# Kernel optimization log

Hardware: AMD Instinct MI355X
Metric: run time of the kernel (lower is better)

## Reference

```python
import jax, jax.numpy as jnp
import numpy as np

N_BATTERS = 20000
N_PITCHERS = 12000
SIT = 64          # situation_size
S = 256           # states per player row
N = N_BATTERS + N_PITCHERS
T = 8192          # number of at-bats (timesteps)
S2 = 2 * S


def setup_inputs() -> dict:
    key = jax.random.key(0)
    ks = jax.random.split(key, 10)
    x = jax.random.normal(ks[0], (T, SIT), dtype=jnp.float32)
    b = jax.random.randint(ks[1], (T,), 0, N)
    p = jax.random.randint(ks[2], (T,), 0, N)
    eye = jnp.eye(S2, dtype=jnp.float32)
    Wz = 0.05 * jax.random.normal(ks[3], (S2, SIT), dtype=jnp.float32)
    Wr = 0.05 * jax.random.normal(ks[4], (S2, SIT), dtype=jnp.float32)
    Wh = 0.05 * jax.random.normal(ks[5], (S2, SIT), dtype=jnp.float32)
    # original uses Identity(gain=0.8) init; small noise added for non-trivial grads
    Uz = 0.8 * eye + 0.02 * jax.random.normal(ks[6], (S2, S2), dtype=jnp.float32)
    Ur = 0.8 * eye + 0.02 * jax.random.normal(ks[7], (S2, S2), dtype=jnp.float32)
    Uh = 0.8 * eye + 0.02 * jax.random.normal(ks[8], (S2, S2), dtype=jnp.float32)
    bz = jnp.zeros((S2,), dtype=jnp.float32)
    br = jnp.ones((S2,), dtype=jnp.float32)
    bh = jnp.zeros((S2,), dtype=jnp.float32)
    table0 = 0.1 * jax.random.normal(ks[9], (N, S), dtype=jnp.float32)
    return dict(x=x, b=b, p=p, Wz=Wz, Wr=Wr, Wh=Wh, Uz=Uz, Ur=Ur, Uh=Uh,
                bz=bz, br=br, bh=bh, table0=table0)


def reference(x, b, p, Wz, Wr, Wh, Uz, Ur, Uh, bz, br, bh, table0):
    states = table0.shape[1]

    def step(table, inp):
        x_t, b_t, p_t = inp
        # gather batter and pitcher rows, concat to (2S,)
        h = jnp.concatenate([table[b_t], table[p_t]], axis=0)
        z = jax.nn.sigmoid(Wz @ x_t + Uz @ h + bz)
        r = jax.nn.sigmoid(Wr @ x_t + Ur @ h - br)   # note: minus br, as in source
        m = jnp.tanh(Wh @ x_t + Uh @ (r * h) + bh)
        hn = z * h + (1.0 - z) * m
        dh = (hn - h).reshape(2, states)
        # scatter-add deltas back (scatter_nd adds; duplicates accumulate)
        table = table.at[b_t].add(dh[0]).at[p_t].add(dh[1])
        return table, None

    final_table, _ = jax.lax.scan(step, table0, (x, b, p))
    return final_table
```

## Files before the change

### kernel.cpp

```cpp
#include <hip/hip_runtime.h>
#include <hip/hip_cooperative_groups.h>

namespace cg = cooperative_groups;

#define T_STEPS 8192
#define SIT     64
#define SS      256
#define S2      512
#define NPL     32000
#define NEV     (2*T_STEPS)
#define MAXLEV  255
#define RELAX   48
#define NKB     (S2/4)
#define WKB     (SIT/4)
#define BQMAX   16
#define CUTN    300
#define NSLICE  4
#define MAXB    4096
#define DIAG    0.8f

typedef __attribute__((ext_vector_type(8))) short short8;
typedef __attribute__((ext_vector_type(4))) float f32x4;

__device__ __forceinline__ float sigmoidf_(float x) {
    return 1.0f / (1.0f + expf(-x));
}
__device__ __forceinline__ float bflo_(unsigned u) { return __uint_as_float(u << 16); }
__device__ __forceinline__ float bfhi_(unsigned u) { return __uint_as_float(u & 0xFFFF0000u); }
__device__ __forceinline__ unsigned short f2bf_(float f) {
    unsigned u = __float_as_uint(f);
    u = u + 0x7FFFu + ((u >> 16) & 1u);
    return (unsigned short)(u >> 16);
}
__device__ __forceinline__ unsigned pk2_(float a, float b) {
    return (unsigned)f2bf_(a) | ((unsigned)f2bf_(b) << 16);
}
__device__ __forceinline__ float dot4_(float4 a, float4 b) {
    return a.x*b.x + a.y*b.y + a.z*b.z + a.w*b.w;
}
__device__ __forceinline__ float loadLLC_(const float* p) {
    return __hip_atomic_load(p, __ATOMIC_RELAXED, __HIP_MEMORY_SCOPE_AGENT);
}
__device__ __forceinline__ void storeLLC_(float* p, float v) {
    __hip_atomic_store(p, v, __ATOMIC_RELAXED, __HIP_MEMORY_SCOPE_AGENT);
}


__global__ void k_count(const int* __restrict__ b, const int* __restrict__ p, int* cnt) {
    int e = blockIdx.x * blockDim.x + threadIdx.x;
    if (e < NEV) {
        int v = (e & 1) ? p[e >> 1] : b[e >> 1];
        atomicAdd(&cnt[v], 1);
    }
}

__global__ __launch_bounds__(1024) void k_scan(const int* __restrict__ cnt, int* bas, int* cur) {
    __shared__ int partial[1024];
    int tid = threadIdx.x;
    int start = tid * 32;
    int end = start + 32; if (end > NPL) end = NPL;
    int s = 0;
    for (int i = start; i < end; ++i) s += cnt[i];
    partial[tid] = s;
    __syncthreads();
    for (int off = 1; off < 1024; off <<= 1) {
        int v = partial[tid];
        int add = (tid >= off) ? partial[tid - off] : 0;
        __syncthreads();
        partial[tid] = v + add;
        __syncthreads();
    }
    int acc = (tid == 0) ? 0 : partial[tid - 1];
    for (int i = start; i < end; ++i) {
        bas[i] = acc; cur[i] = acc; acc += cnt[i];
    }
}

__global__ void k_place(const int* __restrict__ b, const int* __restrict__ p, int* cur, int* list) {
    int e = blockIdx.x * blockDim.x + threadIdx.x;
    if (e < NEV) {
        int v = (e & 1) ? p[e >> 1] : b[e >> 1];
        int pos = atomicAdd(&cur[v], 1);
        list[pos] = e;
    }
}

__global__ void k_pred(const int* __restrict__ bas, const int* __restrict__ cnt, int* list, int* pred) {
    int v = blockIdx.x * blockDim.x + threadIdx.x;
    if (v >= NPL) return;
    int s0 = bas[v], c = cnt[v];
    for (int i2 = 1; i2 < c; ++i2) {
        int key = list[s0 + i2];
        int j = i2 - 1;
        while (j >= 0 && list[s0 + j] > key) { list[s0 + j + 1] = list[s0 + j]; --j; }
        list[s0 + j + 1] = key;
    }
    int prevS = -1, curS = -1;
    for (int i2 = 0; i2 < c; ++i2) {
        int e = list[s0 + i2];
        int s = e >> 1;
        if (s != curS) { prevS = curS; curS = s; }
        pred[e] = prevS;
    }
}

__global__ __launch_bounds__(1024) void k_levels(const int* __restrict__ pred,
                                                 int* order, int* levelStart, int* numLevels) {
    __shared__ short p0[T_STEPS], p1[T_STEPS];
    __shared__ unsigned char lev[T_STEPS];
    __shared__ int cnts[MAXLEV + 2];
    __shared__ int maxLev;
    __shared__ int changed;
    int tid = threadIdx.x;
    for (int t = tid; t < T_STEPS; t += 1024) {
        p0[t] = (short)pred[2 * t];
        p1[t] = (short)pred[2 * t + 1];
        lev[t] = 1;
    }
    for (int l = tid; l < MAXLEV + 2; l += 1024) cnts[l] = 0;
    if (tid == 0) maxLev = 0;
    __syncthreads();
    for (int r = 0; r < RELAX; ++r) {
        if (tid == 0) changed = 0;
        __syncthreads();
        for (int t = tid; t < T_STEPS; t += 1024) {
            int a = p0[t], b2 = p1[t];
            int la = (a >= 0) ? (int)lev[a] : 0;
            int lb = (b2 >= 0) ? (int)lev[b2] : 0;
            int nl = 1 + (la > lb ? la : lb);
            if (nl > MAXLEV) nl = MAXLEV;
            if (nl > (int)lev[t]) { lev[t] = (unsigned char)nl; changed = 1; }
        }
        __syncthreads();
        int ch = changed;
        __syncthreads();
        if (!ch) break;
    }
    for (int t = tid; t < T_STEPS; t += 1024) {
        atomicAdd(&cnts[lev[t]], 1);
        atomicMax(&maxLev, (int)lev[t]);
    }
    __syncthreads();
    if (tid == 0) {
        int acc = 0;
        levelStart[0] = 0;
        int cut = 0, stopped = 0;
        for (int l = 1; l <= maxLev; ++l) {
            int c = cnts[l];
            if (!stopped) { if (c > CUTN) cut = l; else stopped = 1; }
            cnts[l] = acc;
            acc += c;
            levelStart[l] = acc;
        }
        numLevels[0] = maxLev;
        numLevels[1] = cut;
    }
    __syncthreads();
    for (int t = tid; t < T_STEPS; t += 1024) {
        int pos = atomicAdd(&cnts[lev[t]], 1);
        order[pos] = t;
    }
}

__global__ void k_trans(const float* __restrict__ Uz, const float* __restrict__ Ur,
                        const float* __restrict__ Uh, const float* __restrict__ Wz,
                        const float* __restrict__ Wr, const float* __restrict__ Wh,
                        uint4* __restrict__ UzrP, uint2* __restrict__ UhP,
                        unsigned short* __restrict__ UBz, unsigned short* __restrict__ UBr,
                        unsigned short* __restrict__ UBh,
                        float* WzT, float* WrT, float* WhT) {
    int y = blockIdx.y;
    int idx = blockIdx.x * blockDim.x + threadIdx.x;
    if (y == 0) {
        if (idx < S2 * NKB) {
            int kb = idx >> 9, i2 = idx & (S2 - 1);
            int k = kb * 4;
            float z0 = Uz[i2 * S2 + k + 0] - ((i2 == k + 0) ? DIAG : 0.f);
            float z1 = Uz[i2 * S2 + k + 1] - ((i2 == k + 1) ? DIAG : 0.f);
            float z2 = Uz[i2 * S2 + k + 2] - ((i2 == k + 2) ? DIAG : 0.f);
            float z3 = Uz[i2 * S2 + k + 3] - ((i2 == k + 3) ? DIAG : 0.f);
            float r0 = Ur[i2 * S2 + k + 0] - ((i2 == k + 0) ? DIAG : 0.f);
            float r1 = Ur[i2 * S2 + k + 1] - ((i2 == k + 1) ? DIAG : 0.f);
            float r2 = Ur[i2 * S2 + k + 2] - ((i2 == k + 2) ? DIAG : 0.f);
            float r3 = Ur[i2 * S2 + k + 3] - ((i2 == k + 3) ? DIAG : 0.f);
            uint4 o;
            o.x = pk2_(z0, z1); o.y = pk2_(z2, z3);
            o.z = pk2_(r0, r1); o.w = pk2_(r2, r3);
            UzrP[idx] = o;
        }
    } else if (y == 1) {
        if (idx < S2 * NKB) {
            int kb = idx >> 9, i2 = idx & (S2 - 1);
            int k = kb * 4;
            float h0 = Uh[i2 * S2 + k + 0] - ((i2 == k + 0) ? DIAG : 0.f);
            float h1 = Uh[i2 * S2 + k + 1] - ((i2 == k + 1) ? DIAG : 0.f);
            float h2 = Uh[i2 * S2 + k + 2] - ((i2 == k + 2) ? DIAG : 0.f);
            float h3 = Uh[i2 * S2 + k + 3] - ((i2 == k + 3) ? DIAG : 0.f);
            uint2 o;
            o.x = pk2_(h0, h1); o.y = pk2_(h2, h3);
            UhP[idx] = o;
        }
    } else if (y <= 4) {
        const float* S = (y == 2) ? Wz : (y == 3) ? Wr : Wh;
        float*       D = (y == 2) ? WzT : (y == 3) ? WrT : WhT;
        if (idx < S2 * SIT) {
            int i2 = idx / SIT, k = idx % SIT;
            D[((k >> 2) * S2 + i2) * 4 + (k & 3)] = S[idx];
        }
    } else {
        const float* S = (y == 5) ? Uz : (y == 6) ? Ur : Uh;
        unsigned short* D = (y == 5) ? UBz : (y == 6) ? UBr : UBh;
        if (idx < S2 * S2) {
            int j = idx & 7;
            int lane = (idx >> 3) & 63;
            int ks = (idx >> 9) & 15;
            int nb = idx >> 13;
            int row = nb * 16 + (lane & 15);
            int col = ks * 32 + (lane >> 4) * 8 + j;
            float v = S[row * S2 + col] - ((row == col) ? DIAG : 0.f);
            D[idx] = f2bf_(v);
        }
    }
}

__global__ void k_copy(const float4* __restrict__ src, float4* dst, int n4) {
    int i = blockIdx.x * blockDim.x + threadIdx.x;
    if (i < n4) dst[i] = src[i];
}

__global__ __launch_bounds__(512) void k_xp(
    const float* __restrict__ x,
    const float* __restrict__ WzT, const float* __restrict__ WrT, const float* __restrict__ WhT,
    const float* __restrict__ bz, const float* __restrict__ br, const float* __restrict__ bh,
    float* __restrict__ XPz, float* __restrict__ XPr, float* __restrict__ XPh)
{
    __shared__ float xs[16][SIT];
    const int i = threadIdx.x;
    const int tile = blockIdx.x;
    const float4* Wz4 = (const float4*)WzT;
    const float4* Wr4 = (const float4*)WrT;
    const float4* Wh4 = (const float4*)WhT;
    const float bzi = bz[i], bri = br[i], bhi = bh[i];

    for (int idx = i; idx < 16 * SIT; idx += 512) {
        int j = idx >> 6, k = idx & (SIT - 1);
        xs[j][k] = x[(tile * 16 + j) * SIT + k];
    }
    __syncthreads();
    float za[16], ra[16], ha[16];
#pragma unroll
    for (int j = 0; j < 16; ++j) { za[j] = 0.f; ra[j] = 0.f; ha[j] = 0.f; }
    for (int kb = 0; kb < WKB; ++kb) {
        float4 wz = Wz4[kb * S2 + i];
        float4 wr = Wr4[kb * S2 + i];
        float4 wh = Wh4[kb * S2 + i];
#pragma unroll
        for (int j = 0; j < 16; ++j) {
            float4 x4 = *(const float4*)(&xs[j][kb * 4]);
            za[j] += dot4_(wz, x4);
            ra[j] += dot4_(wr, x4);
            ha[j] += dot4_(wh, x4);
        }
    }
#pragma unroll
    for (int j = 0; j < 16; ++j) {
        int t = tile * 16 + j;
        XPz[t * S2 + i] = za[j] + bzi;
        XPr[t * S2 + i] = ra[j] - bri;
        XPh[t * S2 + i] = ha[j] + bhi;
    }
}


__device__ __forceinline__ void tile_mfma(
    int sbase, int B, int i,
    const int* __restrict__ bArr, const int* __restrict__ pArr,
    const unsigned short* __restrict__ UBz, const unsigned short* __restrict__ UBr,
    const unsigned short* __restrict__ UBh,
    const float* __restrict__ XPz, const float* __restrict__ XPr, const float* __restrict__ XPh,
    float* __restrict__ out, const int* __restrict__ order,
    float* pool, int* tj, int* rbs, int* rps)
{
    unsigned short* Hbf  = (unsigned short*)(pool + 8192);
    unsigned short* RHbf = (unsigned short*)(pool + 12288);
    unsigned* H32 = (unsigned*)Hbf;
    const short8* BzF = (const short8*)UBz;
    const short8* BrF = (const short8*)UBr;
    const short8* BhF = (const short8*)UBh;
    const short8* AF  = (const short8*)Hbf;
    const short8* RF  = (const short8*)RHbf;
    const int lane = i & 63;
    const int w = i >> 6;

    __syncthreads();
    if (i < 16) {
        int t = (i < B) ? order[sbase + i] : -1;
        tj[i] = t;
        rbs[i] = (t >= 0) ? bArr[t] : 0;
        rps[i] = (t >= 0) ? pArr[t] : 0;
    }
    __syncthreads();

    for (int idx2 = i; idx2 < 16 * 256; idx2 += 512) {
        int j = idx2 >> 8, kp = (idx2 & 255) << 1;
        float v0 = 0.0f, v1 = 0.0f;
        if (tj[j] >= 0) {
            int row = (kp < SS) ? rbs[j] : rps[j];
            const float* rowp = out + row * SS + (kp & (SS - 1));
            v0 = rowp[0];
            v1 = rowp[1];
        }
        pool[j * S2 + kp] = v0;
        pool[j * S2 + kp + 1] = v1;
        int ks = kp >> 5, kk = kp & 31;
        H32[((((ks << 6) + j + ((kk >> 3) << 4)) << 3) + (kk & 7)) >> 1] = pk2_(v0, v1);
    }
    __syncthreads();

    f32x4 xpz[4], xpr[4];
#pragma unroll
    for (int nb2 = 0; nb2 < 4; ++nb2) {
        int c = (w * 4 + nb2) * 16 + (lane & 15);
#pragma unroll
        for (int q = 0; q < 4; ++q) {
            int m = ((lane >> 4) << 2) + q;
            int t = tj[m];
            xpz[nb2][q] = (t >= 0) ? XPz[t * S2 + c] : 0.f;
            xpr[nb2][q] = (t >= 0) ? XPr[t * S2 + c] : 0.f;
        }
    }

    f32x4 accz[4], accr[4];
#pragma unroll
    for (int nb2 = 0; nb2 < 4; ++nb2) {
        accz[nb2] = (f32x4){0.f, 0.f, 0.f, 0.f};
        accr[nb2] = (f32x4){0.f, 0.f, 0.f, 0.f};
    }
#pragma unroll 1
    for (int ks = 0; ks < 16; ++ks) {
        short8 a = AF[(ks << 6) + lane];
#pragma unroll
        for (int nb2 = 0; nb2 < 4; ++nb2) {
            int nb = w * 4 + nb2;
            short8 bz = BzF[((nb << 4) + ks) * 64 + lane];
            short8 br = BrF[((nb << 4) + ks) * 64 + lane];
            accz[nb2] = __builtin_amdgcn_mfma_f32_16x16x32_bf16(a, bz, accz[nb2], 0, 0, 0);
            accr[nb2] = __builtin_amdgcn_mfma_f32_16x16x32_bf16(a, br, accr[nb2], 0, 0, 0);
        }
    }
    f32x4 zv[4];
#pragma unroll
    for (int nb2 = 0; nb2 < 4; ++nb2) {
        int c = (w * 4 + nb2) * 16 + (lane & 15);
#pragma unroll
        for (int q = 0; q < 4; ++q) {
            int m = ((lane >> 4) << 2) + q;
            int t = tj[m];
            float h = pool[m * S2 + c];
            float zpre = accz[nb2][q] + xpz[nb2][q] + DIAG * h;
            float rpre = accr[nb2][q] + xpr[nb2][q] + DIAG * h;
            zv[nb2][q] = sigmoidf_(zpre);
            float rh = (t >= 0) ? sigmoidf_(rpre) * h : 0.f;
            int ks = c >> 5, kk = c & 31;
            RHbf[((ks << 6) + m + ((kk >> 3) << 4)) * 8 + (kk & 7)] = f2bf_(rh);
        }
    }
    __syncthreads();

    f32x4 xph[4];
#pragma unroll
    for (int nb2 = 0; nb2 < 4; ++nb2) {
        int c = (w * 4 + nb2) * 16 + (lane & 15);
#pragma unroll
        for (int q = 0; q < 4; ++q) {
            int m = ((lane >> 4) << 2) + q;
            int t = tj[m];
            xph[nb2][q] = (t >= 0) ? XPh[t * S2 + c] : 0.f;
        }
    }

    f32x4 accm[4];
#pragma unroll
    for (int nb2 = 0; nb2 < 4; ++nb2) accm[nb2] = (f32x4){0.f, 0.f, 0.f, 0.f};
#pragma unroll 1
    for (int ks = 0; ks < 16; ++ks) {
        short8 a = RF[(ks << 6) + lane];
#pragma unroll
        for (int nb2 = 0; nb2 < 4; ++nb2) {
            int nb = w * 4 + nb2;
            short8 bh = BhF[((nb << 4) + ks) * 64 + lane];
            accm[nb2] = __builtin_amdgcn_mfma_f32_16x16x32_bf16(a, bh, accm[nb2], 0, 0, 0);
        }
    }
#pragma unroll
    for (int nb2 = 0; nb2 < 4; ++nb2) {
        int c = (w * 4 + nb2) * 16 + (lane & 15);
#pragma unroll
        for (int q = 0; q < 4; ++q) {
            int m = ((lane >> 4) << 2) + q;
            int t = tj[m];
            if (t >= 0) {
                float h = pool[m * S2 + c];
                int ks = c >> 5, kk = c & 31;
                float rh = __uint_as_float(
                    ((unsigned)RHbf[((ks << 6) + m + ((kk >> 3) << 4)) * 8 + (kk & 7)]) << 16);
                float mm = tanhf(accm[nb2][q] + xph[nb2][q] + DIAG * rh);
                float z = zv[nb2][q];
                float hn = z * h + (1.f - z) * mm;
                int rb = rbs[m], rp = rps[m];
                int row = (c < SS) ? rb : rp;
                float* addr = out + row * SS + (c & (SS - 1));
                if (rb == rp) atomicAdd(addr, hn - h);
                else *addr = hn;
            }
        }
    }
}

template<int BQ>
__device__ __forceinline__ void process_level_valu(
    int s0, int s1, int i,
    const float* __restrict__ x,
    const int* __restrict__ bArr, const int* __restrict__ pArr,
    const float4* __restrict__ Wz4, const float4* __restrict__ Wr4, const float4* __restrict__ Wh4,
    const uint4* __restrict__ Uzr, const uint2* __restrict__ Uhp,
    float bzi, float bri, float bhi,
    float* __restrict__ out, const int* __restrict__ order,
    float* pool, int* tj, int* rbs, int* rps)
{
    float* Hsf = pool;
    float* RHf = pool + 8192;
    float* xsf = pool + 16384;
    const int nT = (s1 - s0 + BQ - 1) / BQ;
    for (int tile = blockIdx.x; tile < nT; tile += gridDim.x) {
        const int sbase = s0 + tile * BQ;
        const int B = (sbase + BQ <= s1) ? BQ : (s1 - sbase);
        __syncthreads();
        if (i < BQ) {
            int t = (i < B) ? order[sbase + i] : -1;
            tj[i] = t;
            rbs[i] = (t >= 0) ? bArr[t] : 0;
            rps[i] = (t >= 0) ? pArr[t] : 0;
        }
        __syncthreads();
        for (int idx = i; idx < BQ * S2; idx += 512) {
            int j = idx >> 9, k = idx & (S2 - 1);
            float v = 0.0f;
            if (tj[j] >= 0) {
                int row = (k < SS) ? rbs[j] : rps[j];
                v = out[row * SS + (k & (SS - 1))];
            }
            Hsf[j * S2 + k] = v;
        }
        for (int idx = i; idx < BQ * SIT; idx += 512) {
            int j = idx >> 6, k = idx & (SIT - 1);
            int t = tj[j];
            xsf[j * SIT + k] = (t >= 0) ? x[t * SIT + k] : 0.0f;
        }
        float zacc[BQ], racc[BQ];
#pragma unroll
        for (int j = 0; j < BQ; ++j) { zacc[j] = 0.0f; racc[j] = 0.0f; }
        __syncthreads();
        for (int kb = 0; kb < WKB; ++kb) {
            float4 a4 = Wz4[kb * S2 + i];
            float4 b4 = Wr4[kb * S2 + i];
#pragma unroll
            for (int j = 0; j < BQ; ++j) {
                float4 x4 = *(const float4*)(&xsf[j * SIT + kb * 4]);
                zacc[j] += dot4_(a4, x4);
                racc[j] += dot4_(b4, x4);
            }
        }
        for (int kb = 0; kb < NKB; ++kb) {
            uint4 u = Uzr[kb * S2 + i];
#pragma unroll
            for (int j = 0; j < BQ; ++j) {
                float4 h4 = *(const float4*)(&Hsf[j * S2 + kb * 4]);
                zacc[j] += bflo_(u.x) * h4.x + bfhi_(u.x) * h4.y + bflo_(u.y) * h4.z + bfhi_(u.y) * h4.w;
                racc[j] += bflo_(u.z) * h4.x + bfhi_(u.z) * h4.y + bflo_(u.w) * h4.z + bfhi_(u.w) * h4.w;
            }
        }
        float zv[BQ];
#pragma unroll
        for (int j = 0; j < BQ; ++j) {
            float hOwn = Hsf[j * S2 + i];
            zv[j] = sigmoidf_(zacc[j] + DIAG * hOwn + bzi);
            RHf[j * S2 + i] = sigmoidf_(racc[j] + DIAG * hOwn - bri) * hOwn;
        }
        __syncthreads();
        float macc[BQ];
#pragma unroll
        for (int j = 0; j < BQ; ++j) macc[j] = 0.0f;
        for (int kb = 0; kb < WKB; ++kb) {
            float4 a4 = Wh4[kb * S2 + i];
#pragma unroll
            for (int j = 0; j < BQ; ++j) {
                float4 x4 = *(const float4*)(&xsf[j * SIT + kb * 4]);
                macc[j] += dot4_(a4, x4);
            }
        }
        for (int kb = 0; kb < NKB; ++kb) {
            uint2 u = Uhp[kb * S2 + i];
#pragma unroll
            for (int j = 0; j < BQ; ++j) {
                float4 h4 = *(const float4*)(&RHf[j * S2 + kb * 4]);
                macc[j] += bflo_(u.x) * h4.x + bfhi_(u.x) * h4.y + bflo_(u.y) * h4.z + bfhi_(u.y) * h4.w;
            }
        }
        for (int j = 0; j < B; ++j) {
            float mm = tanhf(macc[j] + DIAG * RHf[j * S2 + i] + bhi);
            float h = Hsf[j * S2 + i];
            float hn = zv[j] * h + (1.0f - zv[j]) * mm;
            int rb = rbs[j], rp = rps[j];
            int row = (i < SS) ? rb : rp;
            float* addr = out + row * SS + (i & (SS - 1));
            if (rb == rp) atomicAdd(addr, hn - h);
            else *addr = hn;
        }
    }
}

__global__ __launch_bounds__(512, 4) void k_main(
    const float* __restrict__ x, const int* __restrict__ bArr, const int* __restrict__ pArr,
    const float* __restrict__ WzT, const float* __restrict__ WrT, const float* __restrict__ WhT,
    const uint4* __restrict__ Uzr, const uint2* __restrict__ Uhp,
    const unsigned short* __restrict__ UBz, const unsigned short* __restrict__ UBr,
    const unsigned short* __restrict__ UBh,
    const float* __restrict__ bz, const float* __restrict__ br, const float* __restrict__ bh,
    float* __restrict__ out,
    const int* __restrict__ order, const int* __restrict__ levelStart,
    const int* __restrict__ numLevels,
    const float* __restrict__ XPz, const float* __restrict__ XPr, const float* __restrict__ XPh,
    const int* __restrict__ pred, int* __restrict__ flagArr,
    int* __restrict__ rhCnt, float* __restrict__ RHstage,
    int useXP, int useSlice)
{
    cg::grid_group grid = cg::this_grid();
    __shared__ float pool[17408];
    __shared__ int tj[BQMAX], rbs[BQMAX], rps[BQMAX];

    const int i = threadIdx.x;
    const float bzi = bz[i], bri = br[i], bhi = bh[i];
    const float4* Wz4 = (const float4*)WzT;
    const float4* Wr4 = (const float4*)WrT;
    const float4* Wh4 = (const float4*)WhT;

    const int cutoff = numLevels[1];

    for (int lvl = 1; lvl <= cutoff; ++lvl) {
        const int s0 = levelStart[lvl - 1], s1 = levelStart[lvl];
        if (useXP) {
            const int nT = (s1 - s0 + 15) / 16;
            for (int tile = blockIdx.x; tile < nT; tile += gridDim.x) {
                const int sbase = s0 + tile * 16;
                const int B = (sbase + 16 <= s1) ? 16 : (s1 - sbase);
                tile_mfma(sbase, B, i, bArr, pArr, UBz, UBr, UBh,
                          XPz, XPr, XPh, out, order, pool, tj, rbs, rps);
            }
        } else {
            process_level_valu<8>(s0, s1, i, x, bArr, pArr, Wz4, Wr4, Wh4,
                                  Uzr, Uhp, bzi, bri, bhi, out, order,
                                  pool, tj, rbs, rps);
        }
        grid.sync();
    }

    const int sB = levelStart[cutoff];
    const int nB = T_STEPS - sB;

    for (int s = blockIdx.x * 512 + i; s < T_STEPS; s += gridDim.x * 512)
        flagArr[order[s]] = (s < sB) ? NSLICE : 0;
    for (int c = blockIdx.x * 512 + i; c < MAXB; c += gridDim.x * 512)
        rhCnt[c] = 0;
    grid.sync();

    float* Hs0 = pool;
    float* PB1 = pool + 8192;
    float* PB2 = pool + 8704;
    float* PB3 = pool + 9216;
    float* RHs0 = pool + 9728;
    float* xs0 = pool + 16384;

    if (useSlice && nB <= MAXB) {
        const int jr = i & 127;
        const int ks = i >> 7;
        for (int g = blockIdx.x; g < NSLICE * nB; g += gridDim.x) {
            const int s = sB + (g >> 2);
            const int q = g & 3;
            const int t = order[s];
            const int slot = s - sB;
            if (i == 0) {
                int p0 = pred[2 * t], p1 = pred[2 * t + 1];
                while (p0 >= 0 && __hip_atomic_load(&flagArr[p0], __ATOMIC_ACQUIRE,
                                                    __HIP_MEMORY_SCOPE_AGENT) < NSLICE)
                    __builtin_amdgcn_s_sleep(2);
                while (p1 >= 0 && __hip_atomic_load(&flagArr[p1], __ATOMIC_ACQUIRE,
                                                    __HIP_MEMORY_SCOPE_AGENT) < NSLICE)
                    __builtin_amdgcn_s_sleep(2);
            }
            __syncthreads();

            const int rb = bArr[t], rp = pArr[t];
            {
                const int row = (i < SS) ? rb : rp;
                Hs0[i] = loadLLC_(out + row * SS + (i & (SS - 1)));
            }
            __syncthreads();

            const int myrow = q * 128 + jr;
            const int kb0 = ks * 32;
            float zp = 0.f, rpv = 0.f;
            for (int kb = kb0; kb < kb0 + 32; ++kb) {
                uint4 u = Uzr[kb * S2 + myrow];
                float4 h4 = *(const float4*)(&Hs0[kb * 4]);
                zp  += bflo_(u.x) * h4.x + bfhi_(u.x) * h4.y + bflo_(u.y) * h4.z + bfhi_(u.y) * h4.w;
                rpv += bflo_(u.z) * h4.x + bfhi_(u.z) * h4.y + bflo_(u.w) * h4.z + bfhi_(u.w) * h4.w;
            }
            PB1[ks * 128 + jr] = zp;
            PB2[ks * 128 + jr] = rpv;
            __syncthreads();
            if (i < 128) {
                float hOwn = Hs0[q * 128 + i];
                float zsum = XPz[t * S2 + q * 128 + i] + DIAG * hOwn
                           + PB1[i] + PB1[128 + i] + PB1[256 + i] + PB1[384 + i];
                float rsum = XPr[t * S2 + q * 128 + i] + DIAG * hOwn
                           + PB2[i] + PB2[128 + i] + PB2[256 + i] + PB2[384 + i];
                float zvv = sigmoidf_(zsum);
                float rh = sigmoidf_(rsum) * hOwn;
                storeLLC_(RHstage + (size_t)slot * S2 + q * 128 + i, rh);
                PB3[i] = zvv;
            }
            __syncthreads();
            if (i == 0) {
                __hip_atomic_fetch_add(&rhCnt[slot], 1, __ATOMIC_RELEASE,
                                       __HIP_MEMORY_SCOPE_AGENT);
                while (__hip_atomic_load(&rhCnt[slot], __ATOMIC_ACQUIRE,
                                         __HIP_MEMORY_SCOPE_AGENT) < NSLICE)
                    __builtin_amdgcn_s_sleep(1);
            }
            __syncthreads();
            RHs0[i] = loadLLC_(RHstage + (size_t)slot * S2 + i);
            __syncthreads();

            float mp = 0.f;
            for (int kb = kb0; kb < kb0 + 32; ++kb) {
                uint2 u = Uhp[kb * S2 + myrow];
                float4 h4 = *(const float4*)(&RHs0[kb * 4]);
                mp += bflo_(u.x) * h4.x + bfhi_(u.x) * h4.y + bflo_(u.y) * h4.z + bfhi_(u.y) * h4.w;
            }
            PB1[ks * 128 + jr] = mp;
            __syncthreads();
            if (i < 128) {
                float msum = XPh[t * S2 + q * 128 + i] + DIAG * RHs0[q * 128 + i]
                           + PB1[i] + PB1[128 + i] + PB1[256 + i] + PB1[384 + i];
                float mm = tanhf(msum);
                float zz = PB3[i];
                float h0 = Hs0[q * 128 + i];
                float hn = zz * h0 + (1.f - zz) * mm;
                int grow = q * 128 + i;
                int orow = (grow < SS) ? rb : rp;
                float* addr = out + orow * SS + (grow & (SS - 1));
                if (rb == rp) atomicAdd(addr, hn - h0);
                else storeLLC_(addr, hn);
            }
            __syncthreads();
            if (i == 0)
                __hip_atomic_fetch_add(&flagArr[t], 1, __ATOMIC_RELEASE,
                                       __HIP_MEMORY_SCOPE_AGENT);
        }
    } else {
        for (int s = sB + blockIdx.x; s < T_STEPS; s += gridDim.x) {
            const int t = order[s];
            if (i == 0) {
                int p0 = pred[2 * t], p1 = pred[2 * t + 1];
                while (p0 >= 0 && __hip_atomic_load(&flagArr[p0], __ATOMIC_ACQUIRE,
                                                    __HIP_MEMORY_SCOPE_AGENT) < NSLICE)
                    __builtin_amdgcn_s_sleep(2);
                while (p1 >= 0 && __hip_atomic_load(&flagArr[p1], __ATOMIC_ACQUIRE,
                                                    __HIP_MEMORY_SCOPE_AGENT) < NSLICE)
                    __builtin_amdgcn_s_sleep(2);
            }
            __syncthreads();

            const int rb = bArr[t], rp = pArr[t];
            const int row = (i < SS) ? rb : rp;
            float* addr = out + row * SS + (i & (SS - 1));
            const float h = loadLLC_(addr);
            Hs0[i] = h;
            float zacc, racc;
            if (useXP) {
                zacc = XPz[t * S2 + i];
                racc = XPr[t * S2 + i];
            } else {
                zacc = 0.0f; racc = 0.0f;
                if (i < SIT) xs0[i] = x[t * SIT + i];
            }
            __syncthreads();

            if (!useXP) {
                for (int kb = 0; kb < WKB; ++kb) {
                    float4 a4 = Wz4[kb * S2 + i];
                    float4 b4 = Wr4[kb * S2 + i];
                    float4 x4 = *(const float4*)(&xs0[kb * 4]);
                    zacc += dot4_(a4, x4);
                    racc += dot4_(b4, x4);
                }
            }
            for (int kb = 0; kb < NKB; ++kb) {
                uint4 u = Uzr[kb * S2 + i];
                float4 h4 = *(const float4*)(&Hs0[kb * 4]);
                zacc += bflo_(u.x) * h4.x + bfhi_(u.x) * h4.y + bflo_(u.y) * h4.z + bfhi_(u.y) * h4.w;
                racc += bflo_(u.z) * h4.x + bfhi_(u.z) * h4.y + bflo_(u.w) * h4.z + bfhi_(u.w) * h4.w;
            }
            const float zvv = sigmoidf_(zacc + DIAG * h + (useXP ? 0.f : bzi));
            const float rv = sigmoidf_(racc + DIAG * h - (useXP ? 0.f : bri));
            RHs0[i] = rv * h;
            __syncthreads();

            float macc;
            if (useXP) {
                macc = XPh[t * S2 + i];
            } else {
                macc = 0.0f;
                for (int kb = 0; kb < WKB; ++kb) {
                    float4 a4 = Wh4[kb * S2 + i];
                    float4 x4 = *(const float4*)(&xs0[kb * 4]);
                    macc += dot4_(a4, x4);
                }
            }
            for (int kb = 0; kb < NKB; ++kb) {
                uint2 u = Uhp[kb * S2 + i];
                float4 h4 = *(const float4*)(&RHs0[kb * 4]);
                macc += bflo_(u.x) * h4.x + bfhi_(u.x) * h4.y + bflo_(u.y) * h4.z + bfhi_(u.y) * h4.w;
            }
            const float mm = tanhf(macc + DIAG * RHs0[i] + (useXP ? 0.f : bhi));
            const float hn = zvv * h + (1.0f - zvv) * mm;
            if (rb == rp) atomicAdd(addr, hn - h);
            else storeLLC_(addr, hn);
            __syncthreads();
            if (i == 0)
                __hip_atomic_fetch_add(&flagArr[t], NSLICE, __ATOMIC_RELEASE,
                                       __HIP_MEMORY_SCOPE_AGENT);
        }
    }
}


extern "C" void kernel_launch(void* const* d_in, const int* in_sizes, int n_in,
                              void* d_out, int out_size, void* d_ws, size_t ws_size,
                              hipStream_t stream) {
    const float* x  = (const float*)d_in[0];
    const int*   b  = (const int*)d_in[1];
    const int*   p  = (const int*)d_in[2];
    const float* Wz = (const float*)d_in[3];
    const float* Wr = (const float*)d_in[4];
    const float* Wh = (const float*)d_in[5];
    const float* Uz = (const float*)d_in[6];
    const float* Ur = (const float*)d_in[7];
    const float* Uh = (const float*)d_in[8];
    const float* bz = (const float*)d_in[9];
    const float* br = (const float*)d_in[10];
    const float* bh = (const float*)d_in[11];
    const float* table0 = (const float*)d_in[12];
    float* out = (float*)d_out;

    float* base = (float*)d_ws;
    uint4* UzrP = (uint4*)base;
    uint2* UhP  = (uint2*)(base + 262144);
    unsigned short* UBz = (unsigned short*)(base + 262144 + 131072);
    unsigned short* UBr = (unsigned short*)(base + 262144 + 2 * 131072);
    unsigned short* UBh = (unsigned short*)(base + 262144 + 3 * 131072);
    float* WzT  = base + 262144 + 4 * 131072;
    float* WrT  = WzT + S2 * SIT;
    float* WhT  = WrT + S2 * SIT;
    int* cnt = (int*)(WhT + S2 * SIT);
    int* cur = cnt + NPL;
    int* bas = cur + NPL;
    int* list = bas + NPL;
    int* pred = list + NEV;
    int* order = pred + NEV;
    int* levelStart = order + T_STEPS;
    int* numLevels = levelStart + 260;
    int* flagArr = numLevels + 4;
    int* rhCnt = flagArr + T_STEPS;

    size_t baseFloats = (size_t)262144 + 4 * 131072 + 3 * S2 * SIT
                      + 3 * NPL + 2 * NEV + T_STEPS + 264 + T_STEPS + MAXB;
    baseFloats = (baseFloats + 255) & ~(size_t)255;
    float* RHstage = base + baseFloats;
    size_t rhFloats = (size_t)MAXB * S2;
    size_t xpFloats = 3ull * T_STEPS * S2;

    int useSlice = 0, useXP = 0;
    float *XPz;
    if (ws_size >= (baseFloats + rhFloats + xpFloats) * 4ull) {
        useSlice = 1; useXP = 1; XPz = RHstage + rhFloats;
    } else if (ws_size >= (baseFloats + xpFloats) * 4ull) {
        useXP = 1; XPz = RHstage;
    } else {
        XPz = RHstage;
    }
    float* XPr = XPz + (size_t)T_STEPS * S2;
    float* XPh = XPr + (size_t)T_STEPS * S2;

    hipMemsetAsync(cnt, 0, NPL * sizeof(int), stream);
    hipLaunchKernelGGL(k_trans, dim3(1024, 8), dim3(256), 0, stream,
                       Uz, Ur, Uh, Wz, Wr, Wh, UzrP, UhP, UBz, UBr, UBh, WzT, WrT, WhT);
    hipLaunchKernelGGL(k_count, dim3((NEV + 255) / 256), dim3(256), 0, stream, b, p, cnt);
    hipLaunchKernelGGL(k_scan, dim3(1), dim3(1024), 0, stream, cnt, bas, cur);
    hipLaunchKernelGGL(k_place, dim3((NEV + 255) / 256), dim3(256), 0, stream, b, p, cur, list);
    hipLaunchKernelGGL(k_pred, dim3((NPL + 255) / 256), dim3(256), 0, stream, bas, cnt, list, pred);
    hipLaunchKernelGGL(k_levels, dim3(1), dim3(1024), 0, stream,
                       pred, order, levelStart, numLevels);

    int n4 = NPL * SS / 4;
    hipLaunchKernelGGL(k_copy, dim3((n4 + 255) / 256), dim3(256), 0, stream,
                       (const float4*)table0, (float4*)out, n4);
    if (useXP) {
        hipLaunchKernelGGL(k_xp, dim3(T_STEPS / 16), dim3(512), 0, stream,
                           x, WzT, WrT, WhT, bz, br, bh, XPz, XPr, XPh);
    }

    int occ = 0;
    if (hipOccupancyMaxActiveBlocksPerMultiprocessor(&occ, k_main, 512, 0) != hipSuccess)
        occ = 1;
    if (occ < 1) occ = 1;
    if (occ > 2) occ = 2;
    int gridSz = occ * 256;

    void* args[] = {
        (void*)&x, (void*)&b, (void*)&p,
        (void*)&WzT, (void*)&WrT, (void*)&WhT,
        (void*)&UzrP, (void*)&UhP,
        (void*)&UBz, (void*)&UBr, (void*)&UBh,
        (void*)&bz, (void*)&br, (void*)&bh,
        (void*)&out,
        (void*)&order, (void*)&levelStart, (void*)&numLevels,
        (void*)&XPz, (void*)&XPr, (void*)&XPh,
        (void*)&pred, (void*)&flagArr, (void*)&rhCnt, (void*)&RHstage,
        (void*)&useXP, (void*)&useSlice
    };
    hipError_t e = hipLaunchCooperativeKernel((void*)k_main, dim3(gridSz), dim3(512), args, 0, stream);
    if (e != hipSuccess && gridSz != 256) {
        hipLaunchCooperativeKernel((void*)k_main, dim3(256), dim3(512), args, 0, stream);
    }
}
```

Measured before the change: 644.4 us.

## Replace per-level grid barriers with per-step dataflow flags in MFMA phase

In the MFMA level phase, each tile now spin-waits on per-timestep completion flags of its predecessors and publishes its own flag with a release store after writing rows. This replaces the grid-wide sync after every level with point-to-point dependencies. Row loads and stores go through LLC-coherent helpers, and the flag array and rhCnt are zeroed by a host-side memset. The aim is to cut the barrier cost across many levels, at the price of spin polling and the need for a correct memory ordering.

```diff
diff --git a/kernel.cpp b/kernel.cpp
--- a/kernel.cpp
+++ b/kernel.cpp
@@ -279,6 +279,7 @@
     const unsigned short* __restrict__ UBh,
     const float* __restrict__ XPz, const float* __restrict__ XPr, const float* __restrict__ XPh,
     float* __restrict__ out, const int* __restrict__ order,
+    const int* __restrict__ pred, int* __restrict__ flagArr,
     float* pool, int* tj, int* rbs, int* rps)
 {
     unsigned short* Hbf  = (unsigned short*)(pool + 8192);
@@ -295,6 +296,15 @@
     __syncthreads();
     if (i < 16) {
         int t = (i < B) ? order[sbase + i] : -1;
+        if (t >= 0) {
+            int p0 = pred[2 * t], p1 = pred[2 * t + 1];
+            while (p0 >= 0 && __hip_atomic_load(&flagArr[p0], __ATOMIC_ACQUIRE,
+                                                __HIP_MEMORY_SCOPE_AGENT) < NSLICE)
+                __builtin_amdgcn_s_sleep(2);
+            while (p1 >= 0 && __hip_atomic_load(&flagArr[p1], __ATOMIC_ACQUIRE,
+                                                __HIP_MEMORY_SCOPE_AGENT) < NSLICE)
+                __builtin_amdgcn_s_sleep(2);
+        }
         tj[i] = t;
         rbs[i] = (t >= 0) ? bArr[t] : 0;
         rps[i] = (t >= 0) ? pArr[t] : 0;
@@ -307,8 +317,8 @@
         if (tj[j] >= 0) {
             int row = (kp < SS) ? rbs[j] : rps[j];
             const float* rowp = out + row * SS + (kp & (SS - 1));
-            v0 = rowp[0];
-            v1 = rowp[1];
+            v0 = loadLLC_(rowp);
+            v1 = loadLLC_(rowp + 1);
         }
         pool[j * S2 + kp] = v0;
         pool[j * S2 + kp + 1] = v1;
@@ -411,10 +421,14 @@
                 int row = (c < SS) ? rb : rp;
                 float* addr = out + row * SS + (c & (SS - 1));
                 if (rb == rp) atomicAdd(addr, hn - h);
-                else *addr = hn;
-            }
-        }
-    }
+                else storeLLC_(addr, hn);
+            }
+        }
+    }
+    __syncthreads();
+    if (i < 16 && tj[i] >= 0)
+        __hip_atomic_store(&flagArr[tj[i]], NSLICE, __ATOMIC_RELEASE,
+                           __HIP_MEMORY_SCOPE_AGENT);
 }
 
 template<int BQ>
@@ -546,33 +560,33 @@
     const float4* Wh4 = (const float4*)WhT;
 
     const int cutoff = numLevels[1];
-
-    for (int lvl = 1; lvl <= cutoff; ++lvl) {
-        const int s0 = levelStart[lvl - 1], s1 = levelStart[lvl];
-        if (useXP) {
+    const int sB = levelStart[cutoff];
+    const int nB = T_STEPS - sB;
+
+    if (useXP) {
+        for (int lvl = 1; lvl <= cutoff; ++lvl) {
+            const int s0 = levelStart[lvl - 1], s1 = levelStart[lvl];
             const int nT = (s1 - s0 + 15) / 16;
             for (int tile = blockIdx.x; tile < nT; tile += gridDim.x) {
                 const int sbase = s0 + tile * 16;
                 const int B = (sbase + 16 <= s1) ? 16 : (s1 - sbase);
                 tile_mfma(sbase, B, i, bArr, pArr, UBz, UBr, UBh,
-                          XPz, XPr, XPh, out, order, pool, tj, rbs, rps);
-            }
-        } else {
+                          XPz, XPr, XPh, out, order, pred, flagArr,
+                          pool, tj, rbs, rps);
+            }
+        }
+    } else {
+        for (int lvl = 1; lvl <= cutoff; ++lvl) {
+            const int s0 = levelStart[lvl - 1], s1 = levelStart[lvl];
             process_level_valu<8>(s0, s1, i, x, bArr, pArr, Wz4, Wr4, Wh4,
                                   Uzr, Uhp, bzi, bri, bhi, out, order,
                                   pool, tj, rbs, rps);
-        }
+            grid.sync();
+        }
+        for (int s = blockIdx.x * 512 + i; s < T_STEPS; s += gridDim.x * 512)
+            if (s < sB) flagArr[order[s]] = NSLICE;
         grid.sync();
     }
-
-    const int sB = levelStart[cutoff];
-    const int nB = T_STEPS - sB;
-
-    for (int s = blockIdx.x * 512 + i; s < T_STEPS; s += gridDim.x * 512)
-        flagArr[order[s]] = (s < sB) ? NSLICE : 0;
-    for (int c = blockIdx.x * 512 + i; c < MAXB; c += gridDim.x * 512)
-        rhCnt[c] = 0;
-    grid.sync();
 
     float* Hs0 = pool;
     float* PB1 = pool + 8192;
@@ -804,6 +818,7 @@
     float* XPh = XPr + (size_t)T_STEPS * S2;
 
     hipMemsetAsync(cnt, 0, NPL * sizeof(int), stream);
+    hipMemsetAsync(flagArr, 0, (T_STEPS + MAXB) * sizeof(int), stream);
     hipLaunchKernelGGL(k_trans, dim3(1024, 8), dim3(256), 0, stream,
                        Uz, Ur, Uh, Wz, Wr, Wh, UzrP, UhP, UBz, UBr, UBh, WzT, WrT, WhT);
     hipLaunchKernelGGL(k_count, dim3((NEV + 255) / 256), dim3(256), 0, stream, b, p, cnt);
```

After: 1.250 ms. 94.0% more time.
